# Performance work log

Measured on AMD Instinct MI355X. Metric: run time of the kernel, lower is better.

Reference implementation:

```python
import jax, jax.numpy as jnp
import numpy as np

B, NG, GS, D, L, NDL = 16, 50, 20, 256, 3, 2
N = NG * GS  # 1000


def setup_inputs() -> dict:
    key = jax.random.key(0)
    ks = jax.random.split(key, 8)
    amino_embd = jax.random.normal(ks[0], (B, NG, GS, D), dtype=jnp.float32)
    c = (jax.random.uniform(ks[1], (B, N, N)) < 0.02).astype(jnp.float32)
    prot_contacts = jnp.clip(c + jnp.transpose(c, (0, 2, 1)), 0.0, 1.0)
    # small init for bilinear W (original: random_uniform ~ +/-0.05) keeps exp() stable
    W_list = 0.01 * jax.random.normal(ks[2], (L, D, D), dtype=jnp.float32)
    dense_W = jax.random.normal(ks[3], (L, NDL, D, D), dtype=jnp.float32) / np.sqrt(D)
    dense_b = jnp.zeros((L, NDL, D), dtype=jnp.float32)
    final_W = jax.random.normal(ks[4], (D, D), dtype=jnp.float32) / np.sqrt(D)
    final_b = jnp.zeros((D,), dtype=jnp.float32)
    return {"amino_embd": amino_embd, "prot_contacts": prot_contacts,
            "W_list": W_list, "dense_W": dense_W, "dense_b": dense_b,
            "final_W": final_W, "final_b": final_b}


def reference(amino_embd, prot_contacts, W_list, dense_W, dense_b, final_W, final_b):
    dt = amino_embd.dtype
    eye = jnp.eye(N, dtype=dt)
    A = prot_contacts + eye  # contact map with self loops, [B,N,N]
    x = amino_embd.reshape(B, N, D)
    for l in range(L):
        x0 = x
        # bilinear non-local scores: [B,N,N]
        scores = jnp.einsum('bid,de,bje->bij', x0, W_list[l], x0)
        s = jnp.exp(scores) + jnp.asarray(1e-5, dt) * eye
        s = s * A                                   # mask by contacts + self loop
        s = s / jnp.sum(s, axis=-1, keepdims=True)  # row-normalize
        x = jnp.einsum('bij,bjd->bid', s, x0)       # aggregate
        for dl in range(NDL):
            x = jax.nn.relu(x @ dense_W[l, dl] + dense_b[l, dl])
        x = x + x0  # skip connection
    x = x @ final_W + final_b
    return x.reshape(B, NG, GS, D)
```

## Files before the change

### kernel.cpp

```cpp
#include <hip/hip_runtime.h>

#define BB 16
#define NN 1000
#define DD 256
#define LL 3
#define MAXNZ 256
#define MROWS (BB * NN)
#define SPLIT_SCALE 2048.0f
#define INV_SPLIT 4.8828125e-4f

typedef _Float16 f16x8 __attribute__((ext_vector_type(8)));
typedef _Float16 f16x2 __attribute__((ext_vector_type(2)));
typedef float f32x4 __attribute__((ext_vector_type(4)));

union H8 { f16x8 v; f16x2 p[4]; _Float16 h[8]; int4 i4; };

#if defined(__has_builtin)
#if __has_builtin(__builtin_amdgcn_fdot2)
#define HAS_FDOT2 1
#endif
#endif

__device__ __forceinline__ float dot2f(f16x2 a, f16x2 b, float c) {
#ifdef HAS_FDOT2
    return __builtin_amdgcn_fdot2(a, b, c, false);
#else
    return fmaf((float)a[0], (float)b[0], fmaf((float)a[1], (float)b[1], c));
#endif
}

__global__ __launch_bounds__(256) void setup_all(
    const float* __restrict__ W_list, const float* __restrict__ dense_W,
    const float* __restrict__ final_W,
    _Float16* __restrict__ wt_hi, _Float16* __restrict__ wt_lo,
    const float* __restrict__ x_in,
    _Float16* __restrict__ xh, _Float16* __restrict__ xl,
    const float* __restrict__ contacts,
    int* __restrict__ idx, int* __restrict__ cnt, float* __restrict__ adiag)
{
    __shared__ float T[64][68];
    int bid = blockIdx.x;
    int t = threadIdx.x;

    if (bid < 160) {
        int mat = bid >> 4;
        int tile = bid & 15;
        int tk = (tile >> 2) * 64, tn = (tile & 3) * 64;
        const float* src = (mat < 3) ? (W_list + (size_t)mat * 65536)
                         : (mat < 9) ? (dense_W + (size_t)(mat - 3) * 65536)
                                     : final_W;
        {
            int k = t >> 2, nc = (t & 3) * 16;
            const float* sp = src + (size_t)(tk + k) * 256 + tn + nc;
            *(float4*)&T[k][nc + 0]  = *(const float4*)(sp + 0);
            *(float4*)&T[k][nc + 4]  = *(const float4*)(sp + 4);
            *(float4*)&T[k][nc + 8]  = *(const float4*)(sp + 8);
            *(float4*)&T[k][nc + 12] = *(const float4*)(sp + 12);
        }
        __syncthreads();
        int n = t >> 2, kc = (t & 3) * 16;
        H8 hh0, hh1, ll0, ll1;
        #pragma unroll
        for (int i = 0; i < 16; ++i) {
            float x = T[kc + i][n];
            _Float16 hi = (_Float16)x;
            _Float16 lo = (_Float16)((x - (float)hi) * SPLIT_SCALE);
            if (i < 8) { hh0.h[i] = hi; ll0.h[i] = lo; }
            else       { hh1.h[i - 8] = hi; ll1.h[i - 8] = lo; }
        }
        size_t o = (size_t)mat * 65536 + (size_t)(tn + n) * 256 + tk + kc;
        *(int4*)(wt_hi + o)     = hh0.i4;
        *(int4*)(wt_hi + o + 8) = hh1.i4;
        *(int4*)(wt_lo + o)     = ll0.i4;
        *(int4*)(wt_lo + o + 8) = ll1.i4;
    } else if (bid < 2160) {
        size_t gid = (size_t)(bid - 160) * 256 + t;
        const float* p = x_in + gid * 8;
        float4 a = *(const float4*)p;
        float4 b = *(const float4*)(p + 4);
        float xs[8] = {a.x, a.y, a.z, a.w, b.x, b.y, b.z, b.w};
        H8 hh, ll;
        #pragma unroll
        for (int i = 0; i < 8; ++i) {
            _Float16 h = (_Float16)xs[i];
            hh.h[i] = h;
            ll.h[i] = (_Float16)((xs[i] - (float)h) * SPLIT_SCALE);
        }
        *(int4*)(xh + gid * 8) = hh.i4;
        *(int4*)(xl + gid * 8) = ll.i4;
    } else {
        int wave = (int)(((size_t)(bid - 2160) * 256 + t) >> 6);
        int lane = t & 63;
        int b = wave / NN;
        int i = wave - b * NN;
        const float* row = contacts + (size_t)b * NN * NN + (size_t)i * NN;
        int* out = idx + (size_t)wave * MAXNZ;
        int count = 0;
        for (int j0 = 0; j0 < NN; j0 += 64) {
            int j = j0 + lane;
            float v = (j < NN) ? row[j] : 0.0f;
            bool p = (v != 0.0f) && (j != i);
            unsigned long long bal = __ballot(p);
            if (p) {
                int pre = __popcll(bal & ((1ull << lane) - 1ull));
                out[count + pre] = j;
            }
            count += __popcll(bal);
        }
        if (lane == 0) {
            cnt[wave] = count;
            adiag[wave] = row[i] + 1.0f;
        }
    }
}

__global__ __launch_bounds__(256) void sparse_agg(
    const _Float16* __restrict__ yhi,
    const _Float16* __restrict__ xhi, const _Float16* __restrict__ xlo,
    const int* __restrict__ idx, const int* __restrict__ cnt,
    const float* __restrict__ adiag,
    _Float16* __restrict__ ohi, _Float16* __restrict__ olo)
{
    int bid = blockIdx.x;
    int xcd = bid & 7;
    int chunk = bid >> 3;
    int row = xcd * 2000 + chunk * 4 + (int)(threadIdx.x >> 6);
    row = __builtin_amdgcn_readfirstlane(row);
    int lane = threadIdx.x & 63;
    int g = lane >> 4, s = lane & 15;
    int b = row / NN;

    const _Float16* yp = yhi + (size_t)row * DD + s * 8;
    H8 yh0, yh1;
    yh0.i4 = *(const int4*)yp;
    yh1.i4 = *(const int4*)(yp + 128);

    const _Float16* xph = xhi + (size_t)row * DD + s * 8;
    const _Float16* xpl = xlo + (size_t)row * DD + s * 8;
    H8 xih0, xih1, xil0, xil1;
    xih0.i4 = *(const int4*)xph;       xih1.i4 = *(const int4*)(xph + 128);
    xil0.i4 = *(const int4*)xpl;       xil1.i4 = *(const int4*)(xpl + 128);
    float xi[16];
    #pragma unroll
    for (int u = 0; u < 8; ++u) {
        xi[u]     = fmaf((float)xil0.h[u], INV_SPLIT, (float)xih0.h[u]);
        xi[8 + u] = fmaf((float)xil1.h[u], INV_SPLIT, (float)xih1.h[u]);
    }
    const _Float16* xb = xhi + (size_t)b * NN * DD;

    float p = 0.0f;
    #pragma unroll
    for (int u = 0; u < 8; ++u) {
        p = fmaf((float)yh0.h[u], xi[u], p);
        p = fmaf((float)yh1.h[u], xi[8 + u], p);
    }
    p += __shfl_xor(p, 1); p += __shfl_xor(p, 2);
    p += __shfl_xor(p, 4); p += __shfl_xor(p, 8);
    float wd = (g == 0) ? (__expf(p) + 1e-5f) * adiag[row] : 0.0f;
    float denom = wd;
    float acc[16];
    #pragma unroll
    for (int u = 0; u < 16; ++u) acc[u] = wd * xi[u];

    const int c = cnt[row];
    const int* ip = idx + (size_t)row * MAXNZ;
    const int iters = (c + 3) >> 2;

    int j2;
    H8 v0, v1, n0, n1;
    {
        int ja = (g < c) ? ip[g] : 0;
        int jb = (4 + g < c) ? ip[4 + g] : 0;
        j2 = (8 + g < c) ? ip[8 + g] : 0;
        const _Float16* p0 = xb + (size_t)ja * DD + s * 8;
        v0.i4 = *(const int4*)p0;
        v1.i4 = *(const int4*)(p0 + 128);
        const _Float16* p1 = xb + (size_t)jb * DD + s * 8;
        n0.i4 = *(const int4*)p1;
        n1.i4 = *(const int4*)(p1 + 128);
    }

    for (int t = 0; t < iters; ++t) {
        int k3 = (t + 3) * 4 + g;
        int j3 = (k3 < c) ? ip[k3] : 0;
        H8 m0, m1;
        const _Float16* mp = xb + (size_t)j2 * DD + s * 8;
        m0.i4 = *(const int4*)mp;
        m1.i4 = *(const int4*)(mp + 128);

        bool vok = t * 4 + g < c;
        float q = 0.0f;
        #pragma unroll
        for (int i = 0; i < 4; ++i) q = dot2f(yh0.p[i], v0.p[i], q);
        #pragma unroll
        for (int i = 0; i < 4; ++i) q = dot2f(yh1.p[i], v1.p[i], q);
        q += __shfl_xor(q, 1); q += __shfl_xor(q, 2);
        q += __shfl_xor(q, 4); q += __shfl_xor(q, 8);
        float w = vok ? __expf(q) : 0.0f;
        denom += w;
        #pragma unroll
        for (int u = 0; u < 8; ++u) {
            acc[u]     = fmaf(w, (float)v0.h[u], acc[u]);
            acc[8 + u] = fmaf(w, (float)v1.h[u], acc[8 + u]);
        }

        v0 = n0; v1 = n1;
        n0 = m0; n1 = m1;
        j2 = j3;
    }

#define XG(x) x += __shfl_xor(x, 16); x += __shfl_xor(x, 32);
    XG(denom);
    #pragma unroll
    for (int u = 0; u < 16; ++u) { XG(acc[u]) }
#undef XG

    float inv = 1.0f / denom;
    int half = (g & 1) * 8;
    H8 st;
    #pragma unroll
    for (int i = 0; i < 8; ++i) {
        float x = acc[half + i] * inv;
        _Float16 h = (_Float16)x;
        st.h[i] = (g & 2) ? (_Float16)((x - (float)h) * SPLIT_SCALE) : h;
    }
    _Float16* dst = ((g & 2) ? olo : ohi) + (size_t)row * DD + (g & 1) * 128 + s * 8;
    *(int4*)dst = st.i4;
}

__global__ __launch_bounds__(256, 3) void gemm16(
    const _Float16* __restrict__ Ahi, const _Float16* __restrict__ Alo,
    const _Float16* __restrict__ Bhi, const _Float16* __restrict__ Blo,
    const float* __restrict__ bias,
    const _Float16* __restrict__ Shi, const _Float16* __restrict__ Slo,
    _Float16* __restrict__ Chi, _Float16* __restrict__ Clo,
    float* __restrict__ Cf32, int relu)
{
    __shared__ __align__(16) char smem[32768];
    char* Ah = smem;
    char* Al = smem + 8192;
    char* Bh = smem + 16384;
    char* Bl = smem + 24576;

    int tid = threadIdx.x;
    int mBase = blockIdx.y * 64;
    int nBase = blockIdx.x * 64;

    int r = tid >> 2;
    int kc = (tid & 3) * 16;
    const _Float16* gAh = Ahi + (size_t)(mBase + r) * 256 + kc;
    const _Float16* gAl = Alo + (size_t)(mBase + r) * 256 + kc;
    const _Float16* gBh = Bhi + (size_t)(nBase + r) * 256 + kc;
    const _Float16* gBl = Blo + (size_t)(nBase + r) * 256 + kc;
    int sbase = r * 128 + kc * 2;
    int swz = (r & 7) << 4;

    int l = tid & 63, wv = tid >> 6;
    int wm = (wv & 1) * 32, wn = (wv >> 1) * 32;
    int lr = l & 15, lk = l >> 4;

    f32x4 acc0[2][2] = {};
    f32x4 acc1[2][2] = {};

    int4 rA0, rA1, rA2, rA3, rB0, rB1, rB2, rB3;
#define LOADG(kb) \
    rA0 = *(const int4*)(gAh + (kb));     rA1 = *(const int4*)(gAh + (kb) + 8); \
    rA2 = *(const int4*)(gAl + (kb));     rA3 = *(const int4*)(gAl + (kb) + 8); \
    rB0 = *(const int4*)(gBh + (kb));     rB1 = *(const int4*)(gBh + (kb) + 8); \
    rB2 = *(const int4*)(gBl + (kb));     rB3 = *(const int4*)(gBl + (kb) + 8);

    LOADG(0)

    #pragma unroll
    for (int kb = 0; kb < 256; kb += 64) {
        __syncthreads();
        *(int4*)(Ah + ((sbase +  0) ^ swz)) = rA0;
        *(int4*)(Ah + ((sbase + 16) ^ swz)) = rA1;
        *(int4*)(Al + ((sbase +  0) ^ swz)) = rA2;
        *(int4*)(Al + ((sbase + 16) ^ swz)) = rA3;
        *(int4*)(Bh + ((sbase +  0) ^ swz)) = rB0;
        *(int4*)(Bh + ((sbase + 16) ^ swz)) = rB1;
        *(int4*)(Bl + ((sbase +  0) ^ swz)) = rB2;
        *(int4*)(Bl + ((sbase + 16) ^ swz)) = rB3;
        __syncthreads();

        if (kb < 192) { LOADG(kb + 64) }

        #pragma unroll
        for (int kk = 0; kk < 2; ++kk) {
            int kby = kk * 64 + lk * 16;
            f16x8 fah[2], fal[2], fbh[2], fbl[2];
            #pragma unroll
            for (int mt = 0; mt < 2; ++mt) {
                int ml = wm + mt * 16 + lr;
                int off = (ml * 128 + kby) ^ ((ml & 7) << 4);
                fah[mt] = *(const f16x8*)(Ah + off);
                fal[mt] = *(const f16x8*)(Al + off);
            }
            #pragma unroll
            for (int nt = 0; nt < 2; ++nt) {
                int nl = wn + nt * 16 + lr;
                int off = (nl * 128 + kby) ^ ((nl & 7) << 4);
                fbh[nt] = *(const f16x8*)(Bh + off);
                fbl[nt] = *(const f16x8*)(Bl + off);
            }
            #pragma unroll
            for (int mt = 0; mt < 2; ++mt)
                #pragma unroll
                for (int nt = 0; nt < 2; ++nt) {
                    acc0[mt][nt] = __builtin_amdgcn_mfma_f32_16x16x32_f16(
                        fah[mt], fbh[nt], acc0[mt][nt], 0, 0, 0);
                    acc1[mt][nt] = __builtin_amdgcn_mfma_f32_16x16x32_f16(
                        fah[mt], fbl[nt], acc1[mt][nt], 0, 0, 0);
                    acc1[mt][nt] = __builtin_amdgcn_mfma_f32_16x16x32_f16(
                        fal[mt], fbh[nt], acc1[mt][nt], 0, 0, 0);
                }
        }
    }
#undef LOADG

    #pragma unroll
    for (int mt = 0; mt < 2; ++mt) {
        #pragma unroll
        for (int nt = 0; nt < 2; ++nt) {
            int n = nBase + wn + nt * 16 + lr;
            float bv = bias ? bias[n] : 0.0f;
            #pragma unroll
            for (int q = 0; q < 4; ++q) {
                int m = mBase + wm + mt * 16 + lk * 4 + q;
                size_t o = (size_t)m * 256 + n;
                float v = acc0[mt][nt][q] + acc1[mt][nt][q] * INV_SPLIT + bv;
                if (relu) v = fmaxf(v, 0.0f);
                if (Shi) v += (float)Shi[o] + (float)Slo[o] * INV_SPLIT;
                if (Cf32) {
                    Cf32[o] = v;
                } else {
                    _Float16 hh = (_Float16)v;
                    Chi[o] = hh;
                    Clo[o] = (_Float16)((v - (float)hh) * SPLIT_SCALE);
                }
            }
        }
    }
}

extern "C" void kernel_launch(void* const* d_in, const int* in_sizes, int n_in,
                              void* d_out, int out_size, void* d_ws, size_t ws_size,
                              hipStream_t stream)
{
    const float* x_in     = (const float*)d_in[0];
    const float* contacts = (const float*)d_in[1];
    const float* W_list   = (const float*)d_in[2];
    const float* dense_W  = (const float*)d_in[3];
    const float* dense_b  = (const float*)d_in[4];
    const float* final_W  = (const float*)d_in[5];
    const float* final_b  = (const float*)d_in[6];
    float* out = (float*)d_out;

    char* ws = (char*)d_ws;
    const size_t PL = (size_t)MROWS * DD;
    _Float16* pl[8];
    for (int i = 0; i < 8; ++i) pl[i] = (_Float16*)ws + (size_t)i * PL;
    char* p8 = ws + 8 * PL * sizeof(_Float16);
    int*   idx   = (int*)p8;
    int*   cnt   = (int*)(p8 + (size_t)MROWS * MAXNZ * sizeof(int));
    float* adiag = (float*)((char*)cnt + (size_t)MROWS * sizeof(int));
    _Float16* wt_hi = (_Float16*)((char*)adiag + (size_t)MROWS * sizeof(float));
    _Float16* wt_lo = wt_hi + (size_t)10 * 65536;

    setup_all<<<6160, 256, 0, stream>>>(W_list, dense_W, final_W, wt_hi, wt_lo,
                                        x_in, pl[0], pl[1],
                                        contacts, idx, cnt, adiag);

    dim3 gg(4, MROWS / 64);
    int cur = 0;
    for (int l = 0; l < LL; ++l) {
        int oth = 1 - cur;
        _Float16 *x0h = pl[2 * cur], *x0l = pl[2 * cur + 1];
        _Float16 *yh  = pl[2 * oth], *yl  = pl[2 * oth + 1];
        _Float16 *xah = pl[4], *xal = pl[5];
        _Float16 *xbh = pl[6], *xbl = pl[7];
        gemm16<<<gg, 256, 0, stream>>>(x0h, x0l,
                                       wt_hi + (size_t)l * 65536,
                                       wt_lo + (size_t)l * 65536,
                                       nullptr, nullptr, nullptr,
                                       yh, yl, nullptr, 0);
        sparse_agg<<<MROWS / 4, 256, 0, stream>>>(yh, x0h, x0l, idx, cnt, adiag,
                                                  xah, xal);
        gemm16<<<gg, 256, 0, stream>>>(xah, xal,
                                       wt_hi + (size_t)(3 + l * 2) * 65536,
                                       wt_lo + (size_t)(3 + l * 2) * 65536,
                                       dense_b + (size_t)(l * 2 + 0) * 256,
                                       nullptr, nullptr,
                                       xbh, xbl, nullptr, 1);
        gemm16<<<gg, 256, 0, stream>>>(xbh, xbl,
                                       wt_hi + (size_t)(4 + l * 2) * 65536,
                                       wt_lo + (size_t)(4 + l * 2) * 65536,
                                       dense_b + (size_t)(l * 2 + 1) * 256,
                                       x0h, x0l,
                                       yh, yl, nullptr, 1);
        cur = oth;
    }
    gemm16<<<gg, 256, 0, stream>>>(pl[2 * cur], pl[2 * cur + 1],
                                   wt_hi + (size_t)9 * 65536,
                                   wt_lo + (size_t)9 * 65536,
                                   final_b, nullptr, nullptr,
                                   nullptr, nullptr, out, 0);
}
```

Measured before the change: 303.0 us.

## Stage GEMM epilogue through LDS for vector stores, unroll sparse aggregation by two

The GEMM epilogue now writes accumulators to shared memory, then each thread reads a contiguous 16-element row slice and does vectorized bias, residual loads and 128-bit stores. Before, every element was a scattered 2-byte store. A lo_write flag skips writing the low-half split for the projection output, which sparse_agg only reads as hi. sparse_agg processes two neighbor rows per iteration with independent dot chains, and launch bounds ask for 3 waves. This adds an extra LDS round trip and more registers in sparse_agg.

```diff
diff --git a/kernel.cpp b/kernel.cpp
--- a/kernel.cpp
+++ b/kernel.cpp
@@ -114,7 +114,7 @@
     }
 }
 
-__global__ __launch_bounds__(256) void sparse_agg(
+__global__ __launch_bounds__(256, 3) void sparse_agg(
     const _Float16* __restrict__ yhi,
     const _Float16* __restrict__ xhi, const _Float16* __restrict__ xlo,
     const int* __restrict__ idx, const int* __restrict__ cnt,
@@ -164,49 +164,68 @@
 
     const int c = cnt[row];
     const int* ip = idx + (size_t)row * MAXNZ;
-    const int iters = (c + 3) >> 2;
-
-    int j2;
-    H8 v0, v1, n0, n1;
+    const int iters = (c + 7) >> 3;
+
+    int jA1, jB1;
+    H8 vA0, vA1, vB0, vB1;
     {
         int ja = (g < c) ? ip[g] : 0;
         int jb = (4 + g < c) ? ip[4 + g] : 0;
-        j2 = (8 + g < c) ? ip[8 + g] : 0;
-        const _Float16* p0 = xb + (size_t)ja * DD + s * 8;
-        v0.i4 = *(const int4*)p0;
-        v1.i4 = *(const int4*)(p0 + 128);
-        const _Float16* p1 = xb + (size_t)jb * DD + s * 8;
-        n0.i4 = *(const int4*)p1;
-        n1.i4 = *(const int4*)(p1 + 128);
+        jA1 = (8 + g < c) ? ip[8 + g] : 0;
+        jB1 = (12 + g < c) ? ip[12 + g] : 0;
+        const _Float16* pa = xb + (size_t)ja * DD + s * 8;
+        vA0.i4 = *(const int4*)pa;
+        vA1.i4 = *(const int4*)(pa + 128);
+        const _Float16* pb = xb + (size_t)jb * DD + s * 8;
+        vB0.i4 = *(const int4*)pb;
+        vB1.i4 = *(const int4*)(pb + 128);
     }
 
     for (int t = 0; t < iters; ++t) {
-        int k3 = (t + 3) * 4 + g;
-        int j3 = (k3 < c) ? ip[k3] : 0;
-        H8 m0, m1;
-        const _Float16* mp = xb + (size_t)j2 * DD + s * 8;
-        m0.i4 = *(const int4*)mp;
-        m1.i4 = *(const int4*)(mp + 128);
-
-        bool vok = t * 4 + g < c;
-        float q = 0.0f;
-        #pragma unroll
-        for (int i = 0; i < 4; ++i) q = dot2f(yh0.p[i], v0.p[i], q);
-        #pragma unroll
-        for (int i = 0; i < 4; ++i) q = dot2f(yh1.p[i], v1.p[i], q);
-        q += __shfl_xor(q, 1); q += __shfl_xor(q, 2);
-        q += __shfl_xor(q, 4); q += __shfl_xor(q, 8);
-        float w = vok ? __expf(q) : 0.0f;
-        denom += w;
+        int k2a = (t + 2) * 8 + g;
+        int k2b = k2a + 4;
+        int jA2 = (k2a < c) ? ip[k2a] : 0;
+        int jB2 = (k2b < c) ? ip[k2b] : 0;
+        H8 mA0, mA1, mB0, mB1;
+        const _Float16* pa = xb + (size_t)jA1 * DD + s * 8;
+        mA0.i4 = *(const int4*)pa;
+        mA1.i4 = *(const int4*)(pa + 128);
+        const _Float16* pb = xb + (size_t)jB1 * DD + s * 8;
+        mB0.i4 = *(const int4*)pb;
+        mB1.i4 = *(const int4*)(pb + 128);
+
+        bool vokA = t * 8 + g < c;
+        bool vokB = t * 8 + 4 + g < c;
+
+        float qa0 = 0.0f, qa1 = 0.0f, qb0 = 0.0f, qb1 = 0.0f;
+        #pragma unroll
+        for (int i = 0; i < 4; ++i) {
+            qa0 = dot2f(yh0.p[i], vA0.p[i], qa0);
+            qa1 = dot2f(yh1.p[i], vA1.p[i], qa1);
+            qb0 = dot2f(yh0.p[i], vB0.p[i], qb0);
+            qb1 = dot2f(yh1.p[i], vB1.p[i], qb1);
+        }
+        float qa = qa0 + qa1, qb = qb0 + qb1;
+        qa += __shfl_xor(qa, 1); qb += __shfl_xor(qb, 1);
+        qa += __shfl_xor(qa, 2); qb += __shfl_xor(qb, 2);
+        qa += __shfl_xor(qa, 4); qb += __shfl_xor(qb, 4);
+        qa += __shfl_xor(qa, 8); qb += __shfl_xor(qb, 8);
+        float wa = vokA ? __expf(qa) : 0.0f;
+        float wb = vokB ? __expf(qb) : 0.0f;
+        denom += wa + wb;
         #pragma unroll
         for (int u = 0; u < 8; ++u) {
-            acc[u]     = fmaf(w, (float)v0.h[u], acc[u]);
-            acc[8 + u] = fmaf(w, (float)v1.h[u], acc[8 + u]);
-        }
-
-        v0 = n0; v1 = n1;
-        n0 = m0; n1 = m1;
-        j2 = j3;
+            acc[u]     = fmaf(wa, (float)vA0.h[u], acc[u]);
+            acc[8 + u] = fmaf(wa, (float)vA1.h[u], acc[8 + u]);
+        }
+        #pragma unroll
+        for (int u = 0; u < 8; ++u) {
+            acc[u]     = fmaf(wb, (float)vB0.h[u], acc[u]);
+            acc[8 + u] = fmaf(wb, (float)vB1.h[u], acc[8 + u]);
+        }
+
+        vA0 = mA0; vA1 = mA1; vB0 = mB0; vB1 = mB1;
+        jA1 = jA2; jB1 = jB2;
     }
 
 #define XG(x) x += __shfl_xor(x, 16); x += __shfl_xor(x, 32);
@@ -234,7 +253,7 @@
     const float* __restrict__ bias,
     const _Float16* __restrict__ Shi, const _Float16* __restrict__ Slo,
     _Float16* __restrict__ Chi, _Float16* __restrict__ Clo,
-    float* __restrict__ Cf32, int relu)
+    float* __restrict__ Cf32, int relu, int lo_write)
 {
     __shared__ __align__(16) char smem[32768];
     char* Ah = smem;
@@ -319,25 +338,79 @@
     }
 #undef LOADG
 
-    #pragma unroll
-    for (int mt = 0; mt < 2; ++mt) {
-        #pragma unroll
-        for (int nt = 0; nt < 2; ++nt) {
-            int n = nBase + wn + nt * 16 + lr;
-            float bv = bias ? bias[n] : 0.0f;
+    __syncthreads();
+    float* T = (float*)smem;
+    #pragma unroll
+    for (int mt = 0; mt < 2; ++mt)
+        #pragma unroll
+        for (int nt = 0; nt < 2; ++nt)
             #pragma unroll
             for (int q = 0; q < 4; ++q) {
-                int m = mBase + wm + mt * 16 + lk * 4 + q;
-                size_t o = (size_t)m * 256 + n;
-                float v = acc0[mt][nt][q] + acc1[mt][nt][q] * INV_SPLIT + bv;
-                if (relu) v = fmaxf(v, 0.0f);
-                if (Shi) v += (float)Shi[o] + (float)Slo[o] * INV_SPLIT;
-                if (Cf32) {
-                    Cf32[o] = v;
-                } else {
-                    _Float16 hh = (_Float16)v;
-                    Chi[o] = hh;
-                    Clo[o] = (_Float16)((v - (float)hh) * SPLIT_SCALE);
+                int m = wm + mt * 16 + lk * 4 + q;
+                int n = wn + nt * 16 + lr;
+                T[m * 68 + n] = acc0[mt][nt][q] + acc1[mt][nt][q] * INV_SPLIT;
+            }
+    __syncthreads();
+
+    {
+        int rr = tid >> 2;
+        int c0 = (tid & 3) * 16;
+        int m = mBase + rr;
+        size_t o = (size_t)m * 256 + nBase + c0;
+        float v[16];
+        #pragma unroll
+        for (int i = 0; i < 4; ++i) {
+            float4 f = *(const float4*)&T[rr * 68 + c0 + i * 4];
+            v[i * 4 + 0] = f.x; v[i * 4 + 1] = f.y;
+            v[i * 4 + 2] = f.z; v[i * 4 + 3] = f.w;
+        }
+        if (bias) {
+            #pragma unroll
+            for (int i = 0; i < 4; ++i) {
+                float4 bv = *(const float4*)(bias + nBase + c0 + i * 4);
+                v[i * 4 + 0] += bv.x; v[i * 4 + 1] += bv.y;
+                v[i * 4 + 2] += bv.z; v[i * 4 + 3] += bv.w;
+            }
+        }
+        if (relu) {
+            #pragma unroll
+            for (int i = 0; i < 16; ++i) v[i] = fmaxf(v[i], 0.0f);
+        }
+        if (Shi) {
+            #pragma unroll
+            for (int j = 0; j < 2; ++j) {
+                H8 sh, sl;
+                sh.i4 = *(const int4*)(Shi + o + j * 8);
+                sl.i4 = *(const int4*)(Slo + o + j * 8);
+                #pragma unroll
+                for (int u = 0; u < 8; ++u)
+                    v[j * 8 + u] += fmaf((float)sl.h[u], INV_SPLIT, (float)sh.h[u]);
+            }
+        }
+        if (Cf32) {
+            #pragma unroll
+            for (int i = 0; i < 4; ++i) {
+                *(float4*)(Cf32 + o + i * 4) =
+                    make_float4(v[i * 4], v[i * 4 + 1], v[i * 4 + 2], v[i * 4 + 3]);
+            }
+        } else {
+            #pragma unroll
+            for (int j = 0; j < 2; ++j) {
+                H8 hh;
+                #pragma unroll
+                for (int u = 0; u < 8; ++u) hh.h[u] = (_Float16)v[j * 8 + u];
+                *(int4*)(Chi + o + j * 8) = hh.i4;
+            }
+            if (lo_write) {
+                #pragma unroll
+                for (int j = 0; j < 2; ++j) {
+                    H8 ll;
+                    #pragma unroll
+                    for (int u = 0; u < 8; ++u) {
+                        float x = v[j * 8 + u];
+                        ll.h[u] = (_Float16)((x - (float)(_Float16)x) * SPLIT_SCALE);
+                    }
+                    *(int4*)(Clo + o + j * 8) = ll.i4;
                 }
             }
         }
@@ -384,7 +457,7 @@
                                        wt_hi + (size_t)l * 65536,
                                        wt_lo + (size_t)l * 65536,
                                        nullptr, nullptr, nullptr,
-                                       yh, yl, nullptr, 0);
+                                       yh, yl, nullptr, 0, 0);
         sparse_agg<<<MROWS / 4, 256, 0, stream>>>(yh, x0h, x0l, idx, cnt, adiag,
                                                   xah, xal);
         gemm16<<<gg, 256, 0, stream>>>(xah, xal,
@@ -392,18 +465,18 @@
                                        wt_lo + (size_t)(3 + l * 2) * 65536,
                                        dense_b + (size_t)(l * 2 + 0) * 256,
                                        nullptr, nullptr,
-                                       xbh, xbl, nullptr, 1);
+                                       xbh, xbl, nullptr, 1, 1);
         gemm16<<<gg, 256, 0, stream>>>(xbh, xbl,
                                        wt_hi + (size_t)(4 + l * 2) * 65536,
                                        wt_lo + (size_t)(4 + l * 2) * 65536,
                                        dense_b + (size_t)(l * 2 + 1) * 256,
                                        x0h, x0l,
-                                       yh, yl, nullptr, 1);
+                                       yh, yl, nullptr, 1, 1);
         cur = oth;
     }
     gemm16<<<gg, 256, 0, stream>>>(pl[2 * cur], pl[2 * cur + 1],
                                    wt_hi + (size_t)9 * 65536,
                                    wt_lo + (size_t)9 * 65536,
                                    final_b, nullptr, nullptr,
-                                   nullptr, nullptr, out, 0);
+                                   nullptr, nullptr, out, 0, 0);
 }
```

Result: faster. 286.0 us (-5.6%).
